# Performance work log

Hardware: AMD Instinct MI355X
Metric: run time of the kernel (lower is better)

The kernel has to match this reference:

```python
import jax, jax.numpy as jnp
import numpy as np

D = 1024
H = 16
DH = D // H
NEG = -10000000.0


def setup_inputs() -> dict:
    key = jax.random.key(0)
    ks = jax.random.split(key, 12)
    B, L = 2, 2048
    sc = 0.02
    inp = {
        "q": jax.random.normal(ks[0], (B, L, D), jnp.float32),
        "k": jax.random.normal(ks[1], (B, L, D), jnp.float32),
        "v": jax.random.normal(ks[2], (B, L, D), jnp.float32),
        "attention_mask": jax.random.randint(ks[3], (B, L, L), 0, 2) == 1,
        "head_mask": jnp.ones((1, 1, 1), jnp.float32),
        "Wq": sc * jax.random.normal(ks[4], (D, D), jnp.float32),
        "bq": jnp.zeros((D,), jnp.float32),
        "Wk": sc * jax.random.normal(ks[5], (D, D), jnp.float32),
        "bk": jnp.zeros((D,), jnp.float32),
        "Wv": sc * jax.random.normal(ks[6], (D, D), jnp.float32),
        "bv": jnp.zeros((D,), jnp.float32),
        "Wo": sc * jax.random.normal(ks[7], (D, D), jnp.float32),
        "bo": jnp.zeros((D,), jnp.float32),
    }
    return inp


def reference(q, k, v, attention_mask, head_mask, Wq, bq, Wk, bk, Wv, bv, Wo, bo):
    B, Lq, _ = q.shape
    Lk = k.shape[1]
    # QKV projections (nn.Linear: x @ W.T + b), split into heads
    qh = (q @ Wq.T + bq).reshape(B, Lq, H, DH)  # [B,Lq,H,dh]
    kh = (k @ Wk.T + bk).reshape(B, Lk, H, DH)
    vh = (v @ Wv.T + bv).reshape(B, Lk, H, DH)
    # scores [B,H,Lq,Lk], scaled by 1/sqrt(dh)
    scores = jnp.einsum("bihd,bjhd->bhij", qh, kh) / jnp.sqrt(jnp.float32(DH))
    scores = jnp.where(attention_mask[:, None, :, :], NEG, scores)
    probs = jax.nn.softmax(scores, axis=-1)
    probs = probs * head_mask  # broadcastable head mask (dropout is identity in eval)
    ctx = jnp.einsum("bhij,bjhd->bihd", probs, vh).reshape(B, Lq, D)
    # output linear + residual (Add_and_LN with with_lN=False, eval dropout)
    out = ctx @ Wo.T + bo + q
    return out
```

## Files before the change

### kernel.cpp

```cpp
#include <hip/hip_runtime.h>

typedef unsigned short u16;
typedef unsigned long long u64;
typedef __attribute__((ext_vector_type(4))) float f32x4;
typedef __attribute__((ext_vector_type(8))) short s16x8;
typedef __attribute__((ext_vector_type(4))) short s16x4;
typedef __attribute__((ext_vector_type(4))) unsigned int u32x4;
typedef __attribute__((ext_vector_type(2))) unsigned int u32x2;

#define LDS_LOAD16(gp, lp) __builtin_amdgcn_global_load_lds( \
    (__attribute__((address_space(1))) void*)(gp), \
    (__attribute__((address_space(3))) void*)(lp), 16, 0, 0)

#define MFMA16 __builtin_amdgcn_mfma_f32_16x16x32_bf16

constexpr float L2E = 1.44269504088896340736f;

__device__ __forceinline__ u16 f2bf(float x) {
  unsigned u = __float_as_uint(x);
  u += 0x7FFF + ((u >> 16) & 1);
  return (u16)(u >> 16);
}

__device__ __forceinline__ unsigned cvtpk_bf16(float lo, float hi) {
  unsigned r;
  asm("v_cvt_pk_bf16_f32 %0, %1, %2" : "=v"(r) : "v"(lo), "v"(hi));
  return r;
}

struct ConvArgs {
  const float* src[4];
  u16* dst[4];
  float scale[4];
};

__global__ __launch_bounds__(256) void convert_many(ConvArgs a) {
  const int arr = blockIdx.y;
  const f32x4* src = (const f32x4*)a.src[arr];
  u16* dst = a.dst[arr];
  const float sc = a.scale[arr];
  const int stride = gridDim.x * blockDim.x;
  for (int i = blockIdx.x * blockDim.x + threadIdx.x; i < 262144; i += stride) {
    f32x4 v = src[i];
    s16x4 o;
#pragma unroll
    for (int j = 0; j < 4; ++j) o[j] = (short)f2bf(v[j] * sc);
    *(s16x4*)(dst + (size_t)i * 4) = o;
  }
}

__global__ __launch_bounds__(256) void mask_to_bits(const unsigned int* __restrict__ m32,
                                                    unsigned long long* __restrict__ bits,
                                                    int n) {
  const int i = blockIdx.x * blockDim.x + threadIdx.x;
  const int lane = threadIdx.x & 63;
  unsigned probe = m32[lane];
  bool bytemode = __any(probe > 1u);
  bool v;
  if (bytemode) v = ((const unsigned char*)m32)[i] != 0;
  else          v = m32[i] != 0;
  unsigned long long b = __ballot(v);
  if (lane == 0) bits[i >> 6] = b;
}

struct QkvArgs {
  const float* A[3];
  const u16* B[3];
  const float* bias[3];
  float bscale[3];
  u16* C[3];
};

__global__ __launch_bounds__(256) void gemm_qkv(QkvArgs a) {
  const int z = blockIdx.z;
  const float* __restrict__ A = a.A[z];
  const u16* __restrict__ B = a.B[z];
  const float* __restrict__ bias = a.bias[z];
  const float bscale = a.bscale[z];
  u16* __restrict__ C = a.C[z];

  __shared__ u16 As[2][4096];
  __shared__ u16 Bs[2][4096];
  const int tid = threadIdx.x;
  const int lane = tid & 63;
  const int wave = tid >> 6;
  const int g = lane >> 4, c = lane & 15;
  const int g4 = g * 4;
  const int row0 = blockIdx.x * 128;
  const int col0 = blockIdx.y * 128;
  const int wr = (wave >> 1) * 64, wc = (wave & 1) * 64;

  const int ra = tid >> 2;
  const int cca = (tid & 3) * 8;

  f32x4 acc[4][4] = {};
  f32x4 ar[2][2];

#pragma unroll
  for (int i = 0; i < 2; ++i) {
    ar[i][0] = *(const f32x4*)(A + (size_t)(row0 + i * 64 + ra) * 1024 + cca);
    ar[i][1] = *(const f32x4*)(A + (size_t)(row0 + i * 64 + ra) * 1024 + cca + 4);
  }

  for (int s = 0; s < 32; ++s) {
    const int p = s & 1;
    const int k0 = s * 32;
#pragma unroll
    for (int i = 0; i < 2; ++i) {
      unsigned w0 = cvtpk_bf16(ar[i][0][0], ar[i][0][1]);
      unsigned w1 = cvtpk_bf16(ar[i][0][2], ar[i][0][3]);
      unsigned w2 = cvtpk_bf16(ar[i][1][0], ar[i][1][1]);
      unsigned w3 = cvtpk_bf16(ar[i][1][2], ar[i][1][3]);
      union { u32x4 u; s16x8 v; } w;
      w.u = (u32x4){w0, w1, w2, w3};
      *(s16x8*)(As[p] + (i * 256 + tid) * 8) = w.v;
    }
    if (s < 31) {
#pragma unroll
      for (int i = 0; i < 2; ++i) {
        ar[i][0] = *(const f32x4*)(A + (size_t)(row0 + i * 64 + ra) * 1024 + k0 + 32 + cca);
        ar[i][1] = *(const f32x4*)(A + (size_t)(row0 + i * 64 + ra) * 1024 + k0 + 32 + cca + 4);
      }
    }
#pragma unroll
    for (int i = 0; i < 2; ++i) {
      int e = (i * 256 + tid) * 8;
      LDS_LOAD16(B + (size_t)(col0 + (e >> 5)) * 1024 + k0 + (e & 31), Bs[p] + e);
    }
    __syncthreads();

    s16x8 af[4], bf[4];
#pragma unroll
    for (int m = 0; m < 4; ++m) af[m] = *(const s16x8*)(As[p] + (wr + m * 16 + c) * 32 + g * 8);
#pragma unroll
    for (int n = 0; n < 4; ++n) bf[n] = *(const s16x8*)(Bs[p] + (wc + n * 16 + c) * 32 + g * 8);
#pragma unroll
    for (int m = 0; m < 4; ++m)
#pragma unroll
      for (int n = 0; n < 4; ++n)
        acc[m][n] = MFMA16(bf[n], af[m], acc[m][n], 0, 0, 0);
  }

  f32x4 bv[4];
#pragma unroll
  for (int n = 0; n < 4; ++n) {
    bv[n] = *(const f32x4*)(bias + col0 + wc + n * 16 + g4);
#pragma unroll
    for (int r = 0; r < 4; ++r) bv[n][r] *= bscale;
  }
#pragma unroll
  for (int m = 0; m < 4; ++m)
#pragma unroll
    for (int n = 0; n < 4; ++n) {
      s16x4 o;
#pragma unroll
      for (int r = 0; r < 4; ++r) o[r] = (short)f2bf(acc[m][n][r] + bv[n][r]);
      *(s16x4*)(C + (size_t)(row0 + wr + m * 16 + c) * 1024 + col0 + wc + n * 16 + g4) = o;
    }
}

__global__ __launch_bounds__(256) void gemm_out(const u16* __restrict__ A,
                                                const u16* __restrict__ B,
                                                const float* __restrict__ bias,
                                                const float* __restrict__ resid,
                                                float* __restrict__ C) {
  __shared__ u16 As[64 * 32];
  __shared__ u16 Bs[128 * 32];
  const int tid = threadIdx.x;
  const int lane = tid & 63;
  const int wave = tid >> 6;
  const int g = lane >> 4, c = lane & 15;
  const int g4 = g * 4;
  const int row0 = blockIdx.x * 64;
  const int col0 = blockIdx.y * 128;
  const int wr = (wave >> 1) * 32, wc = (wave & 1) * 64;

  f32x4 acc[2][4] = {};

  for (int k0 = 0; k0 < 1024; k0 += 32) {
    __syncthreads();
    LDS_LOAD16(A + (size_t)(row0 + (tid >> 2)) * 1024 + k0 + (tid & 3) * 8, As + tid * 8);
#pragma unroll
    for (int i = 0; i < 2; ++i) {
      int e = (i * 256 + tid) * 8;
      LDS_LOAD16(B + (size_t)(col0 + (e >> 5)) * 1024 + k0 + (e & 31), Bs + e);
    }
    __syncthreads();
    s16x8 af[2], bf[4];
#pragma unroll
    for (int m = 0; m < 2; ++m) af[m] = *(const s16x8*)(As + (wr + m * 16 + c) * 32 + g * 8);
#pragma unroll
    for (int n = 0; n < 4; ++n) bf[n] = *(const s16x8*)(Bs + (wc + n * 16 + c) * 32 + g * 8);
#pragma unroll
    for (int m = 0; m < 2; ++m)
#pragma unroll
      for (int n = 0; n < 4; ++n)
        acc[m][n] = MFMA16(bf[n], af[m], acc[m][n], 0, 0, 0);
  }

  f32x4 bv[4];
#pragma unroll
  for (int n = 0; n < 4; ++n) bv[n] = *(const f32x4*)(bias + col0 + wc + n * 16 + g4);
#pragma unroll
  for (int m = 0; m < 2; ++m)
#pragma unroll
    for (int n = 0; n < 4; ++n) {
      size_t off = (size_t)(row0 + wr + m * 16 + c) * 1024 + col0 + wc + n * 16 + g4;
      f32x4 rv = *(const f32x4*)(resid + off);
      f32x4 o;
#pragma unroll
      for (int r = 0; r < 4; ++r) o[r] = acc[m][n][r] + bv[n][r] + rv[r];
      *(f32x4*)(C + off) = o;
    }
}

constexpr float NEGV = -10000000.0f;

__global__ __launch_bounds__(256) void attn_kernel(const u16* __restrict__ Qh,
                                                   const u16* __restrict__ Kh,
                                                   const u16* __restrict__ Vh,
                                                   const u64* __restrict__ mbits,
                                                   const float* __restrict__ head_mask,
                                                   u16* __restrict__ ctx) {
  __shared__ u16 Ks[2][4096];
  __shared__ u16 Vt[2][64 * 72];

  const int tid = threadIdx.x;
  const int lane = tid & 63;
  const int wave = tid >> 6;
  const int g = lane >> 4, c = lane & 15;
  const int g4 = g * 4;
  const int wid = (blockIdx.x & 7) * 64 + (blockIdx.x >> 3);
  const int qt = wid & 15;
  const int bh = wid >> 4;
  const int b = bh >> 4;
  const int h = bh & 15;
  const size_t rowbase = (size_t)b * 2048;
  const int D = 1024;

  s16x8 qf[2][2];
#pragma unroll
  for (int s = 0; s < 2; ++s) {
    const int qrow = qt * 128 + s * 64 + wave * 16 + c;
#pragma unroll
    for (int ks = 0; ks < 2; ++ks)
      qf[s][ks] = *(const s16x8*)(Qh + (rowbase + qrow) * D + h * 64 + ks * 32 + g * 8);
  }

  f32x4 accO[2][4] = {};
  float srun[2] = {0.f, 0.f};

  const u64* mrow0 = mbits + (rowbase + qt * 128 + 0 * 64 + wave * 16 + c) * 32;
  const u64* mrow1 = mbits + (rowbase + qt * 128 + 1 * 64 + wave * 16 + c) * 32;

  const int kkK = tid & 63;
  const int aV = tid >> 3;
  const int sV = tid & 7;
  const int dcV = sV * 8;
  const int colV = (2 * aV) ^ (8 * sV);

  const u16* Kbase = Kh + rowbase * D + h * 64;
  const u16* Vbase = Vh + rowbase * D + h * 64;

  s16x8 kreg[2], vreg[2];
#define LOADKV(kb_) { \
    kreg[0] = *(const s16x8*)(Kbase + (size_t)((kb_) + kkK) * D + wave * 8); \
    kreg[1] = *(const s16x8*)(Kbase + (size_t)((kb_) + kkK) * D + (4 + wave) * 8); \
    vreg[0] = *(const s16x8*)(Vbase + (size_t)((kb_) + 2 * aV) * D + dcV); \
    vreg[1] = *(const s16x8*)(Vbase + (size_t)((kb_) + 2 * aV + 1) * D + dcV); }
#define WRITEKV(p_) { \
    *(s16x8*)(Ks[p_] + tid * 8) = kreg[0]; \
    *(s16x8*)(Ks[p_] + 2048 + tid * 8) = kreg[1]; \
    _Pragma("unroll") \
    for (int j = 0; j < 8; ++j) { \
      unsigned pk = (unsigned)(u16)vreg[0][j] | ((unsigned)(u16)vreg[1][j] << 16); \
      *(unsigned*)(Vt[p_] + (dcV + j) * 72 + colV) = pk; } }

  LOADKV(0);
  WRITEKV(0);
  LOADKV(64);
  __syncthreads();

  for (int it = 0; it < 32; ++it) {
    const int p = it & 1;
    if (it < 31) WRITEKV(p ^ 1);
    if (it < 30) LOADKV((it + 2) * 64);

    f32x4 accS[2][4];
#pragma unroll
    for (int t = 0; t < 4; ++t) {
      s16x8 kf0 = *(const s16x8*)(Ks[p] + ((0 + g) * 64 + t * 16 + c) * 8);
      s16x8 kf1 = *(const s16x8*)(Ks[p] + ((4 + g) * 64 + t * 16 + c) * 8);
      f32x4 z0 = {0.f, 0.f, 0.f, 0.f};
      z0 = MFMA16(kf0, qf[0][0], z0, 0, 0, 0);
      accS[0][t] = MFMA16(kf1, qf[0][1], z0, 0, 0, 0);
      f32x4 z1 = {0.f, 0.f, 0.f, 0.f};
      z1 = MFMA16(kf0, qf[1][0], z1, 0, 0, 0);
      accS[1][t] = MFMA16(kf1, qf[1][1], z1, 0, 0, 0);
    }

    s16x8 pa[2][2];
#pragma unroll
    for (int s = 0; s < 2; ++s) {
      u64 mw = (s == 0 ? mrow0 : mrow1)[it];
      u64 sh = mw >> g4;
      unsigned mlo = (unsigned)sh, mhi = (unsigned)(sh >> 32);
      float sp = 0.f;
      unsigned pk0[4], pk1[4];
#pragma unroll
      for (int t = 0; t < 4; ++t) {
        unsigned msrc = (t < 2) ? mlo : mhi;
#pragma unroll
        for (int r = 0; r < 4; ++r) {
          float sv = accS[s][t][r];
          if ((msrc >> ((t & 1) * 16 + r)) & 1) sv = NEGV;
          float pv;
          asm("v_exp_f32 %0, %1" : "=v"(pv) : "v"(sv));
          accS[s][t][r] = pv;
          sp += pv;
        }
        pk0[t] = cvtpk_bf16(accS[s][t][0], accS[s][t][1]);
        pk1[t] = cvtpk_bf16(accS[s][t][2], accS[s][t][3]);
      }
      srun[s] += sp;
#pragma unroll
      for (int ks = 0; ks < 2; ++ks) {
        union { u32x4 u; s16x8 v; } w;
        w.u = (u32x4){pk0[2 * ks], pk1[2 * ks], pk0[2 * ks + 1], pk1[2 * ks + 1]};
        pa[s][ks] = w.v;
      }
    }

#pragma unroll
    for (int d0 = 0; d0 < 4; ++d0) {
      const int dd = d0 * 16 + c;
      const int sw8 = (d0 * 2 + (c >> 3)) * 8;
#pragma unroll
      for (int ks = 0; ks < 2; ++ks) {
        const int base = ks * 32 + g4;
        u32x2 lo = *(const u32x2*)(Vt[p] + dd * 72 + (base ^ sw8));
        u32x2 hi = *(const u32x2*)(Vt[p] + dd * 72 + ((base + 16) ^ sw8));
        union { u32x4 u; s16x8 v; } w;
        w.u = (u32x4){lo[0], lo[1], hi[0], hi[1]};
        accO[0][d0] = MFMA16(w.v, pa[0][ks], accO[0][d0], 0, 0, 0);
        accO[1][d0] = MFMA16(w.v, pa[1][ks], accO[1][d0], 0, 0, 0);
      }
    }
    __syncthreads();
  }

  const float hm = head_mask[0];
#pragma unroll
  for (int s = 0; s < 2; ++s) {
    float tot = srun[s];
    tot += __shfl_xor(tot, 16, 64);
    tot += __shfl_xor(tot, 32, 64);
    float inv = hm / tot;
    const int qrow = qt * 128 + s * 64 + wave * 16 + c;
#pragma unroll
    for (int d0 = 0; d0 < 4; ++d0) {
      s16x4 o;
#pragma unroll
      for (int r = 0; r < 4; ++r) o[r] = (short)f2bf(accO[s][d0][r] * inv);
      *(s16x4*)(ctx + (rowbase + qrow) * D + h * 64 + d0 * 16 + g4) = o;
    }
  }
}

extern "C" void kernel_launch(void* const* d_in, const int* in_sizes, int n_in,
                              void* d_out, int out_size, void* d_ws, size_t ws_size,
                              hipStream_t stream) {
  const float* q  = (const float*)d_in[0];
  const float* k  = (const float*)d_in[1];
  const float* v  = (const float*)d_in[2];
  const void*  am = d_in[3];
  const float* hm = (const float*)d_in[4];
  const float* Wq = (const float*)d_in[5];
  const float* bq = (const float*)d_in[6];
  const float* Wk = (const float*)d_in[7];
  const float* bk = (const float*)d_in[8];
  const float* Wv = (const float*)d_in[9];
  const float* bv = (const float*)d_in[10];
  const float* Wo = (const float*)d_in[11];
  const float* bo = (const float*)d_in[12];

  char* ws = (char*)d_ws;
  const size_t MB = 1024 * 1024;
  u16* Qh  = (u16*)(ws + 0 * MB);
  u16* Kh  = (u16*)(ws + 8 * MB);
  u16* Vh  = (u16*)(ws + 16 * MB);
  u16* wqb = (u16*)(ws + 24 * MB);
  u16* wkb = (u16*)(ws + 26 * MB);
  u16* wvb = (u16*)(ws + 28 * MB);
  u16* wob = (u16*)(ws + 30 * MB);
  unsigned long long* mbits = (unsigned long long*)(ws + 32 * MB);
  u16* ctx = (u16*)(ws + 33 * MB);

  ConvArgs ca;
  ca.src[0] = Wq; ca.dst[0] = wqb; ca.scale[0] = 0.125f * L2E;
  ca.src[1] = Wk; ca.dst[1] = wkb; ca.scale[1] = 1.f;
  ca.src[2] = Wv; ca.dst[2] = wvb; ca.scale[2] = 1.f;
  ca.src[3] = Wo; ca.dst[3] = wob; ca.scale[3] = 1.f;
  convert_many<<<dim3(256, 4), 256, 0, stream>>>(ca);

  mask_to_bits<<<32768, 256, 0, stream>>>((const unsigned int*)am, mbits, 8388608);

  QkvArgs ga;
  ga.A[0] = q; ga.B[0] = wqb; ga.bias[0] = bq; ga.bscale[0] = 0.125f * L2E; ga.C[0] = Qh;
  ga.A[1] = k; ga.B[1] = wkb; ga.bias[1] = bk; ga.bscale[1] = 1.f;          ga.C[1] = Kh;
  ga.A[2] = v; ga.B[2] = wvb; ga.bias[2] = bv; ga.bscale[2] = 1.f;          ga.C[2] = Vh;
  gemm_qkv<<<dim3(32, 8, 3), 256, 0, stream>>>(ga);

  attn_kernel<<<512, 256, 0, stream>>>(Qh, Kh, Vh, mbits, hm, ctx);

  gemm_out<<<dim3(64, 8), 256, 0, stream>>>(ctx, wob, bo, q, (float*)d_out);
}
```

Before: 155.1 us.

## Pre-convert QKV activations to bf16 and double-buffer GEMM LDS loads

When the workspace is large enough, q/k/v are converted to bf16 in the batched convert kernel, and a new QKV GEMM streams bf16 tiles into double-buffered LDS via global_load_lds, prefetching the next K-slice while computing the current one. The output GEMM also gains double buffering with one barrier per step, and both GEMMs swizzle row-block order to improve L2 locality. This trades an extra full pass over the activations (read fp32, write bf16) for a cheaper, overlapped GEMM main loop, and keeps the old fp32-input path as a fallback when the workspace is small.

After: 162.9 us. 5.0% more time.

```diff
diff --git a/kernel.cpp b/kernel.cpp
--- a/kernel.cpp
+++ b/kernel.cpp
@@ -29,18 +29,20 @@
 }
 
 struct ConvArgs {
-  const float* src[4];
-  u16* dst[4];
-  float scale[4];
+  const float* src[7];
+  u16* dst[7];
+  int n4[7];
+  float scale[7];
 };
 
 __global__ __launch_bounds__(256) void convert_many(ConvArgs a) {
   const int arr = blockIdx.y;
   const f32x4* src = (const f32x4*)a.src[arr];
   u16* dst = a.dst[arr];
+  const int n4 = a.n4[arr];
   const float sc = a.scale[arr];
   const int stride = gridDim.x * blockDim.x;
-  for (int i = blockIdx.x * blockDim.x + threadIdx.x; i < 262144; i += stride) {
+  for (int i = blockIdx.x * blockDim.x + threadIdx.x; i < n4; i += stride) {
     f32x4 v = src[i];
     s16x4 o;
 #pragma unroll
@@ -63,7 +65,80 @@
   if (lane == 0) bits[i >> 6] = b;
 }
 
-struct QkvArgs {
+struct QkvArgsB {
+  const u16* A[3];
+  const u16* B[3];
+  const float* bias[3];
+  float bscale[3];
+  u16* C[3];
+};
+
+__global__ __launch_bounds__(256) void gemm_qkv_bf(QkvArgsB a) {
+  const int z = blockIdx.z;
+  const u16* __restrict__ A = a.A[z];
+  const u16* __restrict__ B = a.B[z];
+  const float* __restrict__ bias = a.bias[z];
+  const float bscale = a.bscale[z];
+  u16* __restrict__ C = a.C[z];
+
+  __shared__ u16 As[2][4096];
+  __shared__ u16 Bs[2][4096];
+  const int tid = threadIdx.x;
+  const int lane = tid & 63;
+  const int wave = tid >> 6;
+  const int g = lane >> 4, c = lane & 15;
+  const int g4 = g * 4;
+  const int bx = blockIdx.x;
+  const int row0 = (((bx & 7) << 2) | (bx >> 3)) * 128;
+  const int col0 = blockIdx.y * 128;
+  const int wr = (wave >> 1) * 64, wc = (wave & 1) * 64;
+
+  f32x4 acc[4][4] = {};
+
+#define STAGE_QKV(p_, k0_) { _Pragma("unroll") \
+    for (int i = 0; i < 2; ++i) { \
+      int e = (i * 256 + tid) * 8; \
+      LDS_LOAD16(A + (size_t)(row0 + (e >> 5)) * 1024 + (k0_) + (e & 31), As[p_] + e); \
+      LDS_LOAD16(B + (size_t)(col0 + (e >> 5)) * 1024 + (k0_) + (e & 31), Bs[p_] + e); } }
+
+  STAGE_QKV(0, 0);
+  __syncthreads();
+
+  for (int s = 0; s < 32; ++s) {
+    const int p = s & 1;
+    if (s < 31) STAGE_QKV(p ^ 1, (s + 1) * 32);
+    s16x8 af[4], bf[4];
+#pragma unroll
+    for (int m = 0; m < 4; ++m) af[m] = *(const s16x8*)(As[p] + (wr + m * 16 + c) * 32 + g * 8);
+#pragma unroll
+    for (int n = 0; n < 4; ++n) bf[n] = *(const s16x8*)(Bs[p] + (wc + n * 16 + c) * 32 + g * 8);
+#pragma unroll
+    for (int m = 0; m < 4; ++m)
+#pragma unroll
+      for (int n = 0; n < 4; ++n)
+        acc[m][n] = MFMA16(bf[n], af[m], acc[m][n], 0, 0, 0);
+    __syncthreads();
+  }
+
+  f32x4 bv[4];
+#pragma unroll
+  for (int n = 0; n < 4; ++n) {
+    bv[n] = *(const f32x4*)(bias + col0 + wc + n * 16 + g4);
+#pragma unroll
+    for (int r = 0; r < 4; ++r) bv[n][r] *= bscale;
+  }
+#pragma unroll
+  for (int m = 0; m < 4; ++m)
+#pragma unroll
+    for (int n = 0; n < 4; ++n) {
+      s16x4 o;
+#pragma unroll
+      for (int r = 0; r < 4; ++r) o[r] = (short)f2bf(acc[m][n][r] + bv[n][r]);
+      *(s16x4*)(C + (size_t)(row0 + wr + m * 16 + c) * 1024 + col0 + wc + n * 16 + g4) = o;
+    }
+}
+
+struct QkvArgsF {
   const float* A[3];
   const u16* B[3];
   const float* bias[3];
@@ -71,7 +146,7 @@
   u16* C[3];
 };
 
-__global__ __launch_bounds__(256) void gemm_qkv(QkvArgs a) {
+__global__ __launch_bounds__(256) void gemm_qkv_f32(QkvArgsF a) {
   const int z = blockIdx.z;
   const float* __restrict__ A = a.A[z];
   const u16* __restrict__ B = a.B[z];
@@ -89,13 +164,11 @@
   const int row0 = blockIdx.x * 128;
   const int col0 = blockIdx.y * 128;
   const int wr = (wave >> 1) * 64, wc = (wave & 1) * 64;
-
   const int ra = tid >> 2;
   const int cca = (tid & 3) * 8;
 
   f32x4 acc[4][4] = {};
   f32x4 ar[2][2];
-
 #pragma unroll
   for (int i = 0; i < 2; ++i) {
     ar[i][0] = *(const f32x4*)(A + (size_t)(row0 + i * 64 + ra) * 1024 + cca);
@@ -164,38 +237,44 @@
                                                 const float* __restrict__ bias,
                                                 const float* __restrict__ resid,
                                                 float* __restrict__ C) {
-  __shared__ u16 As[64 * 32];
-  __shared__ u16 Bs[128 * 32];
+  __shared__ u16 As[2][2048];
+  __shared__ u16 Bs[2][4096];
   const int tid = threadIdx.x;
   const int lane = tid & 63;
   const int wave = tid >> 6;
   const int g = lane >> 4, c = lane & 15;
   const int g4 = g * 4;
-  const int row0 = blockIdx.x * 64;
+  const int bx = blockIdx.x;
+  const int row0 = (((bx & 7) << 3) | (bx >> 3)) * 64;
   const int col0 = blockIdx.y * 128;
   const int wr = (wave >> 1) * 32, wc = (wave & 1) * 64;
 
   f32x4 acc[2][4] = {};
 
-  for (int k0 = 0; k0 < 1024; k0 += 32) {
-    __syncthreads();
-    LDS_LOAD16(A + (size_t)(row0 + (tid >> 2)) * 1024 + k0 + (tid & 3) * 8, As + tid * 8);
-#pragma unroll
-    for (int i = 0; i < 2; ++i) {
-      int e = (i * 256 + tid) * 8;
-      LDS_LOAD16(B + (size_t)(col0 + (e >> 5)) * 1024 + k0 + (e & 31), Bs + e);
-    }
-    __syncthreads();
+#define STAGE_OUT(p_, k0_) { \
+    LDS_LOAD16(A + (size_t)(row0 + (tid >> 2)) * 1024 + (k0_) + (tid & 3) * 8, As[p_] + tid * 8); \
+    _Pragma("unroll") \
+    for (int i = 0; i < 2; ++i) { \
+      int e = (i * 256 + tid) * 8; \
+      LDS_LOAD16(B + (size_t)(col0 + (e >> 5)) * 1024 + (k0_) + (e & 31), Bs[p_] + e); } }
+
+  STAGE_OUT(0, 0);
+  __syncthreads();
+
+  for (int s = 0; s < 32; ++s) {
+    const int p = s & 1;
+    if (s < 31) STAGE_OUT(p ^ 1, (s + 1) * 32);
     s16x8 af[2], bf[4];
 #pragma unroll
-    for (int m = 0; m < 2; ++m) af[m] = *(const s16x8*)(As + (wr + m * 16 + c) * 32 + g * 8);
-#pragma unroll
-    for (int n = 0; n < 4; ++n) bf[n] = *(const s16x8*)(Bs + (wc + n * 16 + c) * 32 + g * 8);
+    for (int m = 0; m < 2; ++m) af[m] = *(const s16x8*)(As[p] + (wr + m * 16 + c) * 32 + g * 8);
+#pragma unroll
+    for (int n = 0; n < 4; ++n) bf[n] = *(const s16x8*)(Bs[p] + (wc + n * 16 + c) * 32 + g * 8);
 #pragma unroll
     for (int m = 0; m < 2; ++m)
 #pragma unroll
       for (int n = 0; n < 4; ++n)
         acc[m][n] = MFMA16(bf[n], af[m], acc[m][n], 0, 0, 0);
+    __syncthreads();
   }
 
   f32x4 bv[4];
@@ -386,32 +465,71 @@
 
   char* ws = (char*)d_ws;
   const size_t MB = 1024 * 1024;
-  u16* Qh  = (u16*)(ws + 0 * MB);
-  u16* Kh  = (u16*)(ws + 8 * MB);
-  u16* Vh  = (u16*)(ws + 16 * MB);
-  u16* wqb = (u16*)(ws + 24 * MB);
-  u16* wkb = (u16*)(ws + 26 * MB);
-  u16* wvb = (u16*)(ws + 28 * MB);
-  u16* wob = (u16*)(ws + 30 * MB);
-  unsigned long long* mbits = (unsigned long long*)(ws + 32 * MB);
-  u16* ctx = (u16*)(ws + 33 * MB);
-
-  ConvArgs ca;
-  ca.src[0] = Wq; ca.dst[0] = wqb; ca.scale[0] = 0.125f * L2E;
-  ca.src[1] = Wk; ca.dst[1] = wkb; ca.scale[1] = 1.f;
-  ca.src[2] = Wv; ca.dst[2] = wvb; ca.scale[2] = 1.f;
-  ca.src[3] = Wo; ca.dst[3] = wob; ca.scale[3] = 1.f;
-  convert_many<<<dim3(256, 4), 256, 0, stream>>>(ca);
-
-  mask_to_bits<<<32768, 256, 0, stream>>>((const unsigned int*)am, mbits, 8388608);
-
-  QkvArgs ga;
-  ga.A[0] = q; ga.B[0] = wqb; ga.bias[0] = bq; ga.bscale[0] = 0.125f * L2E; ga.C[0] = Qh;
-  ga.A[1] = k; ga.B[1] = wkb; ga.bias[1] = bk; ga.bscale[1] = 1.f;          ga.C[1] = Kh;
-  ga.A[2] = v; ga.B[2] = wvb; ga.bias[2] = bv; ga.bscale[2] = 1.f;          ga.C[2] = Vh;
-  gemm_qkv<<<dim3(32, 8, 3), 256, 0, stream>>>(ga);
-
-  attn_kernel<<<512, 256, 0, stream>>>(Qh, Kh, Vh, mbits, hm, ctx);
-
-  gemm_out<<<dim3(64, 8), 256, 0, stream>>>(ctx, wob, bo, q, (float*)d_out);
-}
+  const bool big = ws_size >= 58 * MB;
+
+  if (big) {
+    u16* qb  = (u16*)(ws + 0 * MB);
+    u16* kb  = (u16*)(ws + 8 * MB);
+    u16* vb  = (u16*)(ws + 16 * MB);
+    u16* wqb = (u16*)(ws + 24 * MB);
+    u16* wkb = (u16*)(ws + 26 * MB);
+    u16* wvb = (u16*)(ws + 28 * MB);
+    u16* wob = (u16*)(ws + 30 * MB);
+    u16* Qh  = (u16*)(ws + 32 * MB);
+    u16* Kh  = (u16*)(ws + 40 * MB);
+    u16* Vh  = (u16*)(ws + 48 * MB);
+    unsigned long long* mbits = (unsigned long long*)(ws + 56 * MB);
+    u16* ctx = qb;
+
+    ConvArgs ca;
+    ca.src[0] = q;  ca.dst[0] = qb;  ca.n4[0] = 1048576; ca.scale[0] = 1.f;
+    ca.src[1] = k;  ca.dst[1] = kb;  ca.n4[1] = 1048576; ca.scale[1] = 1.f;
+    ca.src[2] = v;  ca.dst[2] = vb;  ca.n4[2] = 1048576; ca.scale[2] = 1.f;
+    ca.src[3] = Wq; ca.dst[3] = wqb; ca.n4[3] = 262144;  ca.scale[3] = 0.125f * L2E;
+    ca.src[4] = Wk; ca.dst[4] = wkb; ca.n4[4] = 262144;  ca.scale[4] = 1.f;
+    ca.src[5] = Wv; ca.dst[5] = wvb; ca.n4[5] = 262144;  ca.scale[5] = 1.f;
+    ca.src[6] = Wo; ca.dst[6] = wob; ca.n4[6] = 262144;  ca.scale[6] = 1.f;
+    convert_many<<<dim3(512, 7), 256, 0, stream>>>(ca);
+
+    mask_to_bits<<<32768, 256, 0, stream>>>((const unsigned int*)am, mbits, 8388608);
+
+    QkvArgsB ga;
+    ga.A[0] = qb; ga.B[0] = wqb; ga.bias[0] = bq; ga.bscale[0] = 0.125f * L2E; ga.C[0] = Qh;
+    ga.A[1] = kb; ga.B[1] = wkb; ga.bias[1] = bk; ga.bscale[1] = 1.f;          ga.C[1] = Kh;
+    ga.A[2] = vb; ga.B[2] = wvb; ga.bias[2] = bv; ga.bscale[2] = 1.f;          ga.C[2] = Vh;
+    gemm_qkv_bf<<<dim3(32, 8, 3), 256, 0, stream>>>(ga);
+
+    attn_kernel<<<512, 256, 0, stream>>>(Qh, Kh, Vh, mbits, hm, ctx);
+
+    gemm_out<<<dim3(64, 8), 256, 0, stream>>>(ctx, wob, bo, q, (float*)d_out);
+  } else {
+    u16* Qh  = (u16*)(ws + 0 * MB);
+    u16* Kh  = (u16*)(ws + 8 * MB);
+    u16* Vh  = (u16*)(ws + 16 * MB);
+    u16* wqb = (u16*)(ws + 24 * MB);
+    u16* wkb = (u16*)(ws + 26 * MB);
+    u16* wvb = (u16*)(ws + 28 * MB);
+    u16* wob = (u16*)(ws + 30 * MB);
+    unsigned long long* mbits = (unsigned long long*)(ws + 32 * MB);
+    u16* ctx = (u16*)(ws + 33 * MB);
+
+    ConvArgs ca;
+    ca.src[0] = Wq; ca.dst[0] = wqb; ca.n4[0] = 262144; ca.scale[0] = 0.125f * L2E;
+    ca.src[1] = Wk; ca.dst[1] = wkb; ca.n4[1] = 262144; ca.scale[1] = 1.f;
+    ca.src[2] = Wv; ca.dst[2] = wvb; ca.n4[2] = 262144; ca.scale[2] = 1.f;
+    ca.src[3] = Wo; ca.dst[3] = wob; ca.n4[3] = 262144; ca.scale[3] = 1.f;
+    convert_many<<<dim3(256, 4), 256, 0, stream>>>(ca);
+
+    mask_to_bits<<<32768, 256, 0, stream>>>((const unsigned int*)am, mbits, 8388608);
+
+    QkvArgsF ga;
+    ga.A[0] = q; ga.B[0] = wqb; ga.bias[0] = bq; ga.bscale[0] = 0.125f * L2E; ga.C[0] = Qh;
+    ga.A[1] = k; ga.B[1] = wkb; ga.bias[1] = bk; ga.bscale[1] = 1.f;          ga.C[1] = Kh;
+    ga.A[2] = v; ga.B[2] = wvb; ga.bias[2] = bv; ga.bscale[2] = 1.f;          ga.C[2] = Vh;
+    gemm_qkv_f32<<<dim3(32, 8, 3), 256, 0, stream>>>(ga);
+
+    attn_kernel<<<512, 256, 0, stream>>>(Qh, Kh, Vh, mbits, hm, ctx);
+
+    gemm_out<<<dim3(64, 8), 256, 0, stream>>>(ctx, wob, bo, q, (float*)d_out);
+  }
+}
```
